# Performance work log

Hardware: AMD Instinct MI355X
Metric: run time of the kernel (lower is better)

The kernel has to match this reference:

```python
import jax, jax.numpy as jnp
import numpy as np

ALPHA = 0.2      # LeakyReLU negative slope
NEG_BIG = -9e15  # mask value from the original module


def setup_inputs() -> dict:
    key = jax.random.key(0)
    kx, ka, kW, ka1, ka2, kb = jax.random.split(key, 6)
    B, N, F_in, F_out = 8, 2048, 256, 128
    x = jax.random.normal(kx, (B, N, F_in), dtype=jnp.float32)
    adj = (jax.random.uniform(ka, (B, N, N)) < 0.1).astype(jnp.float32)
    adj = adj.at[:, jnp.arange(N), jnp.arange(N)].set(1.0)
    # parameters (xavier-uniform-ish scaling)
    W = jax.random.normal(kW, (F_out, F_in), dtype=jnp.float32) * np.sqrt(2.0 / (F_in + F_out))
    a1 = jax.random.normal(ka1, (F_out,), dtype=jnp.float32) * np.sqrt(2.0 / (2 * F_out + 1))
    a2 = jax.random.normal(ka2, (F_out,), dtype=jnp.float32) * np.sqrt(2.0 / (2 * F_out + 1))
    a_b = jax.random.normal(kb, (1,), dtype=jnp.float32) * 0.01
    return {"x": x, "adj": adj, "W": W, "a1": a1, "a2": a2, "a_b": a_b}


def reference(x, adj, W, a1, a2, a_b):
    # h = W(input): [B, N, F_out]
    h = jnp.einsum('bnf,of->bno', x, W)
    # a([h_i, h_j]) == a1.h_i + a2.h_j + bias  (exact decomposition of the concat)
    s1 = h @ a1  # [B, N] contribution of row-repeated node i
    s2 = h @ a2  # [B, N] contribution of tiled node j
    e = jax.nn.leaky_relu(s1[:, :, None] + s2[:, None, :] + a_b[0], negative_slope=ALPHA)  # [B,N,N]
    att = jnp.where(adj > 0, e, NEG_BIG)
    att = jax.nn.softmax(att, axis=1)  # softmax over dim=1, as in the original
    # dropout is a no-op in eval mode
    att = att * adj
    h_prime = jnp.einsum('bij,bjo->bio', att, h)
    return jax.nn.elu(h_prime)  # concat=True -> ELU
```

## Files before the change

### kernel.cpp

```cpp
#include <hip/hip_runtime.h>
#include <stdint.h>

typedef unsigned int  uint32;
typedef unsigned long long u64;

#define L2E 1.44269504088896340736f

typedef float f32x4 __attribute__((ext_vector_type(4)));
typedef short bf16x8 __attribute__((ext_vector_type(8)));

__device__ __forceinline__ unsigned short f2bf(float f){
  uint32 u = __float_as_uint(f);
  u += 0x7fffu + ((u >> 16) & 1u);
  return (unsigned short)(u >> 16);
}


__global__ __launch_bounds__(256) void k_h(const float* __restrict__ x,
                                           const float* __restrict__ W,
                                           const float* __restrict__ a1,
                                           const float* __restrict__ a2,
                                           const float* __restrict__ ab,
                                           float* __restrict__ h,
                                           float* __restrict__ E1,
                                           float* __restrict__ E2p){
  __shared__ unsigned short xs[2][64][72];
  __shared__ unsigned short wsm[2][128][72];
  const int tid = threadIdx.x;
  const int wv = tid >> 6, lane = tid & 63;
  const int r = lane & 15, kg = lane >> 4;
  const int row0 = blockIdx.x * 64;

  f32x4 acc[8];
  #pragma unroll
  for (int of = 0; of < 8; ++of) acc[of] = (f32x4){0.f,0.f,0.f,0.f};

  for (int kc = 0; kc < 4; ++kc){
    if (kc) __syncthreads();
    #pragma unroll
    for (int it = 0; it < 4; ++it){
      int idx = tid + it * 256;
      int row = idx >> 4, f = (idx & 15) * 4;
      float4 v = *(const float4*)(x + (size_t)(row0 + row) * 256 + kc * 64 + f);
      ushort4 hi, lo;
      { unsigned short hh = f2bf(v.x); float rr = v.x - __uint_as_float(((uint32)hh)<<16); hi.x = hh; lo.x = f2bf(rr); }
      { unsigned short hh = f2bf(v.y); float rr = v.y - __uint_as_float(((uint32)hh)<<16); hi.y = hh; lo.y = f2bf(rr); }
      { unsigned short hh = f2bf(v.z); float rr = v.z - __uint_as_float(((uint32)hh)<<16); hi.z = hh; lo.z = f2bf(rr); }
      { unsigned short hh = f2bf(v.w); float rr = v.w - __uint_as_float(((uint32)hh)<<16); hi.w = hh; lo.w = f2bf(rr); }
      *(ushort4*)&xs[0][row][f] = hi;
      *(ushort4*)&xs[1][row][f] = lo;
    }
    #pragma unroll
    for (int it = 0; it < 8; ++it){
      int idx = tid + it * 256;
      int o = idx >> 4, f = (idx & 15) * 4;
      float4 v = *(const float4*)(W + (size_t)o * 256 + kc * 64 + f);
      ushort4 hi, lo;
      { unsigned short hh = f2bf(v.x); float rr = v.x - __uint_as_float(((uint32)hh)<<16); hi.x = hh; lo.x = f2bf(rr); }
      { unsigned short hh = f2bf(v.y); float rr = v.y - __uint_as_float(((uint32)hh)<<16); hi.y = hh; lo.y = f2bf(rr); }
      { unsigned short hh = f2bf(v.z); float rr = v.z - __uint_as_float(((uint32)hh)<<16); hi.z = hh; lo.z = f2bf(rr); }
      { unsigned short hh = f2bf(v.w); float rr = v.w - __uint_as_float(((uint32)hh)<<16); hi.w = hh; lo.w = f2bf(rr); }
      *(ushort4*)&wsm[0][o][f] = hi;
      *(ushort4*)&wsm[1][o][f] = lo;
    }
    __syncthreads();
    #pragma unroll
    for (int kk = 0; kk < 2; ++kk){
      bf16x8 ah = *(const bf16x8*)&xs[0][wv*16 + r][kk*32 + kg*8];
      bf16x8 al = *(const bf16x8*)&xs[1][wv*16 + r][kk*32 + kg*8];
      #pragma unroll
      for (int of = 0; of < 8; ++of){
        bf16x8 bh = *(const bf16x8*)&wsm[0][of*16 + r][kk*32 + kg*8];
        bf16x8 bl = *(const bf16x8*)&wsm[1][of*16 + r][kk*32 + kg*8];
        acc[of] = __builtin_amdgcn_mfma_f32_16x16x32_bf16(ah, bh, acc[of], 0, 0, 0);
        acc[of] = __builtin_amdgcn_mfma_f32_16x16x32_bf16(ah, bl, acc[of], 0, 0, 0);
        acc[of] = __builtin_amdgcn_mfma_f32_16x16x32_bf16(al, bh, acc[of], 0, 0, 0);
      }
    }
  }
  #pragma unroll
  for (int of = 0; of < 8; ++of)
    #pragma unroll
    for (int q = 0; q < 4; ++q)
      h[(size_t)(row0 + wv*16 + kg*4 + q) * 128 + of*16 + r] = acc[of][q];

  float p1[4] = {0,0,0,0}, p2[4] = {0,0,0,0};
  #pragma unroll
  for (int of = 0; of < 8; ++of){
    float w1 = a1[of*16 + r], w2 = a2[of*16 + r];
    #pragma unroll
    for (int q = 0; q < 4; ++q){
      p1[q] = fmaf(acc[of][q], w1, p1[q]);
      p2[q] = fmaf(acc[of][q], w2, p2[q]);
    }
  }
  #pragma unroll
  for (int off = 8; off; off >>= 1)
    #pragma unroll
    for (int q = 0; q < 4; ++q){
      p1[q] += __shfl_xor(p1[q], off);
      p2[q] += __shfl_xor(p2[q], off);
    }
  if (r == 0){
    float abv = ab[0];
    #pragma unroll
    for (int q = 0; q < 4; ++q){
      int row = row0 + wv*16 + kg*4 + q;
      E1[row] = p1[q] * L2E;
      int bb = row >> 11, j = row & 2047;
      int kp = (j & ~255) + (j & 3) * 64 + ((j & 255) >> 2);
      E2p[bb * 2048 + kp] = (p2[q] + abv) * L2E;
    }
  }
}

__global__ __launch_bounds__(256) void k_dm(const float* __restrict__ adj,
                                            const float* __restrict__ E1,
                                            const float* __restrict__ E2p,
                                            float* __restrict__ denomP,
                                            u64* __restrict__ mask){
  __shared__ float red[4][256];
  const int b = blockIdx.z, Q = blockIdx.x, ic = blockIdx.y;
  const int wv = threadIdx.x >> 6, lane = threadIdx.x & 63;
  const int Jbase = Q * 256;
  const int row0 = ic * 64 + wv * 16;
  const int grow0 = b * 2048 + row0;

  const f32x4* ap = (const f32x4*)(adj + (size_t)grow0 * 2048 + Jbase) + lane;
  u64* mp = mask + (size_t)grow0 * 32 + Q * 4;

  float e2v[4];
  #pragma unroll
  for (int p = 0; p < 4; ++p)
    e2v[p] = E2p[b * 2048 + Q * 256 + p * 64 + lane];

  float e1r[16];
  #pragma unroll
  for (int q = 0; q < 4; ++q){
    float4 t = *(const float4*)(E1 + grow0 + q * 4);
    e1r[q*4+0] = t.x; e1r[q*4+1] = t.y; e1r[q*4+2] = t.z; e1r[q*4+3] = t.w;
  }

  float ds0 = 0.f, ds1 = 0.f, ds2 = 0.f, ds3 = 0.f;

  #pragma unroll
  for (int rr = 0; rr < 16; ++rr){
    f32x4 av = __builtin_nontemporal_load(ap + (size_t)rr * 512);
    const float e1 = e1r[rr];
    float t0 = e1 + e2v[0]; t0 = fmaxf(t0, 0.2f * t0);
    float t1 = e1 + e2v[1]; t1 = fmaxf(t1, 0.2f * t1);
    float t2 = e1 + e2v[2]; t2 = fmaxf(t2, 0.2f * t2);
    float t3 = e1 + e2v[3]; t3 = fmaxf(t3, 0.2f * t3);
    ds0 = fmaf(av[0], __builtin_amdgcn_exp2f(t0), ds0);
    ds1 = fmaf(av[1], __builtin_amdgcn_exp2f(t1), ds1);
    ds2 = fmaf(av[2], __builtin_amdgcn_exp2f(t2), ds2);
    ds3 = fmaf(av[3], __builtin_amdgcn_exp2f(t3), ds3);
    u64 b0 = __ballot(av[0] != 0.f);
    u64 b1 = __ballot(av[1] != 0.f);
    u64 b2 = __ballot(av[2] != 0.f);
    u64 b3 = __ballot(av[3] != 0.f);
    if (lane == 0){
      ulonglong2* dst = (ulonglong2*)(mp + (size_t)rr * 32);
      dst[0] = (ulonglong2){b0, b1};
      dst[1] = (ulonglong2){b2, b3};
    }
  }

  *(float4*)&red[wv][lane * 4] = (float4){ds0, ds1, ds2, ds3};
  __syncthreads();
  const int t = threadIdx.x;
  denomP[(size_t)ic * 16384 + b * 2048 + Jbase + t] = red[0][t] + red[1][t] + red[2][t] + red[3][t];
}

__global__ __launch_bounds__(256) void k_gt(const float* __restrict__ h,
                                            const float* __restrict__ denomP,
                                            unsigned short* __restrict__ gTp){
  __shared__ float hl[8464];
  __shared__ float rrec[256];
  const int b = blockIdx.z, Q = blockIdx.x, ot = blockIdx.y;
  const int o0 = ot * 32;
  const int tid = threadIdx.x;

  {
    float d = 0.f;
    #pragma unroll
    for (int icc = 0; icc < 32; ++icc)
      d += denomP[(size_t)icc * 16384 + b * 2048 + Q * 256 + tid];
    rrec[tid] = 1.0f / d;
  }
  __syncthreads();

  #pragma unroll
  for (int it = 0; it < 8; ++it){
    int idx = tid + it * 256;
    int j = idx >> 3, f = idx & 7;
    float4 v = *(const float4*)(h + (size_t)(b * 2048 + Q * 256 + j) * 128 + o0 + f * 4);
    float rc = rrec[j];
    int base = j * 33 + (j >> 4) + f * 4;
    hl[base + 0] = v.x * rc;
    hl[base + 1] = v.y * rc;
    hl[base + 2] = v.z * rc;
    hl[base + 3] = v.w * rc;
  }
  __syncthreads();

  const int u  = tid & 127;
  const int fh = tid >> 7;
  const int lane = u >> 1;
  const int e0 = (u & 1) * 4;
  const int orow_r = lane & 15;
  const int kgrp = lane >> 4;
  #pragma unroll
  for (int it = 0; it < 8; ++it){
    int f  = it * 2 + fh;
    int kb = f >> 1, sl = f & 1;
    int orow = sl * 16 + orow_r;
    int klb = kb * 32 + kgrp * 8 + e0;
    ushort4 uu;
    { int kl = klb + 0; int jl = 4 * (kl & 63) + (kl >> 6); uu.x = f2bf(hl[jl * 33 + (jl >> 4) + orow]); }
    { int kl = klb + 1; int jl = 4 * (kl & 63) + (kl >> 6); uu.y = f2bf(hl[jl * 33 + (jl >> 4) + orow]); }
    { int kl = klb + 2; int jl = 4 * (kl & 63) + (kl >> 6); uu.z = f2bf(hl[jl * 33 + (jl >> 4) + orow]); }
    { int kl = klb + 3; int jl = 4 * (kl & 63) + (kl >> 6); uu.w = f2bf(hl[jl * 33 + (jl >> 4) + orow]); }
    size_t dst = ((size_t)((b * 64 + Q * 8 + kb) * 8 + (ot * 2 + sl))) * 512 + lane * 8 + e0;
    *(ushort4*)(gTp + dst) = uu;
  }
}

__global__ __launch_bounds__(256) void k_main(const float* __restrict__ E1,
                                              const float* __restrict__ E2p,
                                              const uint32* __restrict__ mask32,
                                              const unsigned short* __restrict__ gTp,
                                              float* __restrict__ out){
  __shared__ float cmb[4][32][129];
  const int b  = blockIdx.y;
  const int ib = blockIdx.x;
  const int wv = threadIdx.x >> 6, lane = threadIdx.x & 63;
  const int r  = lane & 15, kg = lane >> 4;
  const int gi0 = b * 2048 + ib * 32 + r;
  const float e1_0 = E1[gi0];
  const float e1_1 = E1[gi0 + 16];
  const uint32* m0 = mask32 + (size_t)gi0 * 64;
  const uint32* m1 = mask32 + (size_t)(gi0 + 16) * 64;

  f32x4 acc[2][8];
  #pragma unroll
  for (int si = 0; si < 2; ++si)
    #pragma unroll
    for (int so = 0; so < 8; ++so)
      acc[si][so] = (f32x4){0.f, 0.f, 0.f, 0.f};

  const int k0 = wv * 512, k1 = k0 + 512;
  for (int kk = k0; kk < k1; kk += 32){
    const int j0 = kk + kg * 8;
    const float4 eA = *(const float4*)(E2p + b * 2048 + j0);
    const float4 eB = *(const float4*)(E2p + b * 2048 + j0 + 4);
    const uint32 bits0 = (m0[kk >> 5] >> (kg * 8)) & 0xffu;
    const uint32 bits1 = (m1[kk >> 5] >> (kg * 8)) & 0xffu;
    float e2v[8] = {eA.x, eA.y, eA.z, eA.w, eB.x, eB.y, eB.z, eB.w};

    union { uint32 u[4]; bf16x8 v; } af0, af1;
    #pragma unroll
    for (int p = 0; p < 4; ++p){
      {
        float t0 = e1_0 + e2v[2*p];     t0 = fmaxf(t0, 0.2f * t0);
        float t1 = e1_0 + e2v[2*p+1];   t1 = fmaxf(t1, 0.2f * t1);
        float x0 = ((bits0 >> (2*p))   & 1u) ? __builtin_amdgcn_exp2f(t0) : 0.f;
        float x1 = ((bits0 >> (2*p+1)) & 1u) ? __builtin_amdgcn_exp2f(t1) : 0.f;
        uint32 u0 = __float_as_uint(x0); u0 = (u0 + 0x7fffu + ((u0 >> 16) & 1u)) >> 16;
        uint32 u1 = __float_as_uint(x1); u1 = (u1 + 0x7fffu + ((u1 >> 16) & 1u)) & 0xffff0000u;
        af0.u[p] = u0 | u1;
      }
      {
        float t0 = e1_1 + e2v[2*p];     t0 = fmaxf(t0, 0.2f * t0);
        float t1 = e1_1 + e2v[2*p+1];   t1 = fmaxf(t1, 0.2f * t1);
        float x0 = ((bits1 >> (2*p))   & 1u) ? __builtin_amdgcn_exp2f(t0) : 0.f;
        float x1 = ((bits1 >> (2*p+1)) & 1u) ? __builtin_amdgcn_exp2f(t1) : 0.f;
        uint32 u0 = __float_as_uint(x0); u0 = (u0 + 0x7fffu + ((u0 >> 16) & 1u)) >> 16;
        uint32 u1 = __float_as_uint(x1); u1 = (u1 + 0x7fffu + ((u1 >> 16) & 1u)) & 0xffff0000u;
        af1.u[p] = u0 | u1;
      }
    }
    const unsigned short* gk = gTp + ((size_t)(b * 64 + (kk >> 5)) * 8) * 512 + lane * 8;
    #pragma unroll
    for (int so = 0; so < 8; ++so){
      bf16x8 bfr = *(const bf16x8*)(gk + so * 512);
      acc[0][so] = __builtin_amdgcn_mfma_f32_16x16x32_bf16(af0.v, bfr, acc[0][so], 0, 0, 0);
      acc[1][so] = __builtin_amdgcn_mfma_f32_16x16x32_bf16(af1.v, bfr, acc[1][so], 0, 0, 0);
    }
  }

  #pragma unroll
  for (int si = 0; si < 2; ++si)
    #pragma unroll
    for (int so = 0; so < 8; ++so)
      #pragma unroll
      for (int q = 0; q < 4; ++q){
        int il = si * 16 + kg * 4 + q;
        int o  = so * 16 + r;
        cmb[wv][il][o] = acc[si][so][q];
      }
  __syncthreads();
  for (int e = threadIdx.x; e < 4096; e += 256){
    int i = e >> 7, o = e & 127;
    float v = cmb[0][i][o] + cmb[1][i][o] + cmb[2][i][o] + cmb[3][i][o];
    float res = v > 0.f ? v : (__builtin_amdgcn_exp2f(v * L2E) - 1.0f);
    out[(size_t)(b * 2048 + ib * 32 + i) * 128 + o] = res;
  }
}

extern "C" void kernel_launch(void* const* d_in, const int* in_sizes, int n_in,
                              void* d_out, int out_size, void* d_ws, size_t ws_size,
                              hipStream_t stream){
  const float* x   = (const float*)d_in[0];
  const float* adj = (const float*)d_in[1];
  const float* W   = (const float*)d_in[2];
  const float* a1  = (const float*)d_in[3];
  const float* a2  = (const float*)d_in[4];
  const float* ab  = (const float*)d_in[5];
  float* out = (float*)d_out;

  const size_t WS_NEEDED = 19005440;
  if (ws_size < WS_NEEDED) return;

  char* ws = (char*)d_ws;
  float* h      = (float*)(ws);
  float* E1     = (float*)(ws + 8388608);
  float* E2p    = (float*)(ws + 8454144);
  float* denomP = (float*)(ws + 8519680);
  u64*   mask   = (u64*)  (ws + 10616832);
  unsigned short* gTp = (unsigned short*)(ws + 14811136);

  k_h  <<<256, 256, 0, stream>>>(x, W, a1, a2, ab, h, E1, E2p);
  k_dm <<<dim3(8, 32, 8), 256, 0, stream>>>(adj, E1, E2p, denomP, mask);
  k_gt <<<dim3(8, 4, 8), 256, 0, stream>>>(h, denomP, gTp);
  k_main<<<dim3(64, 8), 256, 0, stream>>>(E1, E2p, (const uint32*)mask, gTp, out);
}
```

Measured before the change: 77.92 us.

## Give each k_dm block 256 rows and batch adjacency loads eight at a time

The k_dm column-sum/mask kernel now has each wave process 64 rows instead of 16, so the grid shrinks from 32 to 8 row-chunks and the partial-denominator buffer and its reduction in k_gt shrink to match. Adjacency rows are loaded in groups of eight per loop iteration to keep more memory requests in flight, and the nontemporal load hint is dropped. This cuts the partial-sum traffic and the k_gt reduction work, but leaves 512 blocks instead of 2048 to cover the large adjacency read, which may lower memory-level parallelism.

```diff
diff --git a/kernel.cpp b/kernel.cpp
--- a/kernel.cpp
+++ b/kernel.cpp
@@ -123,46 +123,44 @@
   const int b = blockIdx.z, Q = blockIdx.x, ic = blockIdx.y;
   const int wv = threadIdx.x >> 6, lane = threadIdx.x & 63;
   const int Jbase = Q * 256;
-  const int row0 = ic * 64 + wv * 16;
-  const int grow0 = b * 2048 + row0;
-
-  const f32x4* ap = (const f32x4*)(adj + (size_t)grow0 * 2048 + Jbase) + lane;
-  u64* mp = mask + (size_t)grow0 * 32 + Q * 4;
+  const int row0 = ic * 256 + wv * 64;
+
+  const float* e1p = E1 + b * 2048 + row0;
+  const f32x4* ap = (const f32x4*)(adj + (size_t)(b * 2048 + row0) * 2048 + Jbase) + lane;
+  u64* mp = mask + (size_t)(b * 2048 + row0) * 32 + Q * 4;
 
   float e2v[4];
   #pragma unroll
   for (int p = 0; p < 4; ++p)
     e2v[p] = E2p[b * 2048 + Q * 256 + p * 64 + lane];
 
-  float e1r[16];
-  #pragma unroll
-  for (int q = 0; q < 4; ++q){
-    float4 t = *(const float4*)(E1 + grow0 + q * 4);
-    e1r[q*4+0] = t.x; e1r[q*4+1] = t.y; e1r[q*4+2] = t.z; e1r[q*4+3] = t.w;
-  }
-
   float ds0 = 0.f, ds1 = 0.f, ds2 = 0.f, ds3 = 0.f;
 
-  #pragma unroll
-  for (int rr = 0; rr < 16; ++rr){
-    f32x4 av = __builtin_nontemporal_load(ap + (size_t)rr * 512);
-    const float e1 = e1r[rr];
-    float t0 = e1 + e2v[0]; t0 = fmaxf(t0, 0.2f * t0);
-    float t1 = e1 + e2v[1]; t1 = fmaxf(t1, 0.2f * t1);
-    float t2 = e1 + e2v[2]; t2 = fmaxf(t2, 0.2f * t2);
-    float t3 = e1 + e2v[3]; t3 = fmaxf(t3, 0.2f * t3);
-    ds0 = fmaf(av[0], __builtin_amdgcn_exp2f(t0), ds0);
-    ds1 = fmaf(av[1], __builtin_amdgcn_exp2f(t1), ds1);
-    ds2 = fmaf(av[2], __builtin_amdgcn_exp2f(t2), ds2);
-    ds3 = fmaf(av[3], __builtin_amdgcn_exp2f(t3), ds3);
-    u64 b0 = __ballot(av[0] != 0.f);
-    u64 b1 = __ballot(av[1] != 0.f);
-    u64 b2 = __ballot(av[2] != 0.f);
-    u64 b3 = __ballot(av[3] != 0.f);
-    if (lane == 0){
-      ulonglong2* dst = (ulonglong2*)(mp + (size_t)rr * 32);
-      dst[0] = (ulonglong2){b0, b1};
-      dst[1] = (ulonglong2){b2, b3};
+  for (int r0 = 0; r0 < 64; r0 += 8){
+    f32x4 av[8];
+    #pragma unroll
+    for (int u = 0; u < 8; ++u)
+      av[u] = ap[(size_t)(r0 + u) * 512];
+    #pragma unroll
+    for (int u = 0; u < 8; ++u){
+      const float e1 = e1p[r0 + u];
+      float t0 = e1 + e2v[0]; t0 = fmaxf(t0, 0.2f * t0);
+      float t1 = e1 + e2v[1]; t1 = fmaxf(t1, 0.2f * t1);
+      float t2 = e1 + e2v[2]; t2 = fmaxf(t2, 0.2f * t2);
+      float t3 = e1 + e2v[3]; t3 = fmaxf(t3, 0.2f * t3);
+      ds0 = fmaf(av[u][0], __builtin_amdgcn_exp2f(t0), ds0);
+      ds1 = fmaf(av[u][1], __builtin_amdgcn_exp2f(t1), ds1);
+      ds2 = fmaf(av[u][2], __builtin_amdgcn_exp2f(t2), ds2);
+      ds3 = fmaf(av[u][3], __builtin_amdgcn_exp2f(t3), ds3);
+      u64 b0 = __ballot(av[u][0] != 0.f);
+      u64 b1 = __ballot(av[u][1] != 0.f);
+      u64 b2 = __ballot(av[u][2] != 0.f);
+      u64 b3 = __ballot(av[u][3] != 0.f);
+      if (lane == 0){
+        ulonglong2* dst = (ulonglong2*)(mp + (size_t)(r0 + u) * 32);
+        dst[0] = (ulonglong2){b0, b1};
+        dst[1] = (ulonglong2){b2, b3};
+      }
     }
   }
 
@@ -184,7 +182,7 @@
   {
     float d = 0.f;
     #pragma unroll
-    for (int icc = 0; icc < 32; ++icc)
+    for (int icc = 0; icc < 8; ++icc)
       d += denomP[(size_t)icc * 16384 + b * 2048 + Q * 256 + tid];
     rrec[tid] = 1.0f / d;
   }
@@ -319,7 +317,7 @@
   const float* ab  = (const float*)d_in[5];
   float* out = (float*)d_out;
 
-  const size_t WS_NEEDED = 19005440;
+  const size_t WS_NEEDED = 17432576;
   if (ws_size < WS_NEEDED) return;
 
   char* ws = (char*)d_ws;
@@ -327,11 +325,11 @@
   float* E1     = (float*)(ws + 8388608);
   float* E2p    = (float*)(ws + 8454144);
   float* denomP = (float*)(ws + 8519680);
-  u64*   mask   = (u64*)  (ws + 10616832);
-  unsigned short* gTp = (unsigned short*)(ws + 14811136);
+  u64*   mask   = (u64*)  (ws + 9043968);
+  unsigned short* gTp = (unsigned short*)(ws + 13238272);
 
   k_h  <<<256, 256, 0, stream>>>(x, W, a1, a2, ab, h, E1, E2p);
-  k_dm <<<dim3(8, 32, 8), 256, 0, stream>>>(adj, E1, E2p, denomP, mask);
+  k_dm <<<dim3(8, 8, 8), 256, 0, stream>>>(adj, E1, E2p, denomP, mask);
   k_gt <<<dim3(8, 4, 8), 256, 0, stream>>>(h, denomP, gTp);
   k_main<<<dim3(64, 8), 256, 0, stream>>>(E1, E2p, (const uint32*)mask, gTp, out);
 }
```

Measured after the change: 68.68 us, median of 2. 1.13x faster.

## Split adjacency bitmask build from denominator; compute column sums from bitmask

Applied to the files above, without the earlier changes.

Replaces the fused adjacency-scan kernel with two kernels. A pure mask builder streams the dense adjacency once and writes the bitmask. A new denominator kernel then reads the compact bitmask plus E1/E2 to compute the column softmax sums in fewer partial chunks. The mask kernel launches before the projection kernel, so the dense adj read no longer waits on the projection. In exchange it adds a launch and recomputes exp for every (i,j) pair from the bitmask. It also changes the partial-sum layout that the gather kernel reads.

```diff
diff --git a/kernel.cpp b/kernel.cpp
--- a/kernel.cpp
+++ b/kernel.cpp
@@ -15,6 +15,32 @@
   return (unsigned short)(u >> 16);
 }
 
+
+__global__ __launch_bounds__(256) void k_mask(const float* __restrict__ adj,
+                                              u64* __restrict__ mask){
+  const int bid = blockIdx.x;
+  const int wv = threadIdx.x >> 6, lane = threadIdx.x & 63;
+  const int row0 = bid * 16 + wv * 4;
+  const f32x4* ap = (const f32x4*)(adj + (size_t)row0 * 2048) + lane;
+  u64* mp = mask + (size_t)row0 * 32;
+
+  #pragma unroll
+  for (int rr = 0; rr < 4; ++rr){
+    #pragma unroll
+    for (int c = 0; c < 8; ++c){
+      f32x4 av = ap[(size_t)rr * 512 + c * 64];
+      u64 b0 = __ballot(av[0] != 0.f);
+      u64 b1 = __ballot(av[1] != 0.f);
+      u64 b2 = __ballot(av[2] != 0.f);
+      u64 b3 = __ballot(av[3] != 0.f);
+      if (lane == 0){
+        ulonglong2* dst = (ulonglong2*)(mp + (size_t)rr * 32 + c * 4);
+        dst[0] = (ulonglong2){b0, b1};
+        dst[1] = (ulonglong2){b2, b3};
+      }
+    }
+  }
+}
 
 __global__ __launch_bounds__(256) void k_h(const float* __restrict__ x,
                                            const float* __restrict__ W,
@@ -114,66 +140,33 @@
   }
 }
 
-__global__ __launch_bounds__(256) void k_dm(const float* __restrict__ adj,
-                                            const float* __restrict__ E1,
-                                            const float* __restrict__ E2p,
-                                            float* __restrict__ denomP,
-                                            u64* __restrict__ mask){
-  __shared__ float red[4][256];
-  const int b = blockIdx.z, Q = blockIdx.x, ic = blockIdx.y;
+__global__ __launch_bounds__(256) void k_den(const u64* __restrict__ mask,
+                                             const float* __restrict__ E1,
+                                             const float* __restrict__ E2p,
+                                             float* __restrict__ denomK){
+  const int wg = blockIdx.x, ch = blockIdx.y, b = blockIdx.z;
   const int wv = threadIdx.x >> 6, lane = threadIdx.x & 63;
-  const int Jbase = Q * 256;
-  const int row0 = ic * 64 + wv * 16;
-  const int grow0 = b * 2048 + row0;
-
-  const f32x4* ap = (const f32x4*)(adj + (size_t)grow0 * 2048 + Jbase) + lane;
-  u64* mp = mask + (size_t)grow0 * 32 + Q * 4;
-
-  float e2v[4];
-  #pragma unroll
-  for (int p = 0; p < 4; ++p)
-    e2v[p] = E2p[b * 2048 + Q * 256 + p * 64 + lane];
-
-  float e1r[16];
-  #pragma unroll
-  for (int q = 0; q < 4; ++q){
-    float4 t = *(const float4*)(E1 + grow0 + q * 4);
-    e1r[q*4+0] = t.x; e1r[q*4+1] = t.y; e1r[q*4+2] = t.z; e1r[q*4+3] = t.w;
-  }
-
-  float ds0 = 0.f, ds1 = 0.f, ds2 = 0.f, ds3 = 0.f;
-
-  #pragma unroll
-  for (int rr = 0; rr < 16; ++rr){
-    f32x4 av = __builtin_nontemporal_load(ap + (size_t)rr * 512);
-    const float e1 = e1r[rr];
-    float t0 = e1 + e2v[0]; t0 = fmaxf(t0, 0.2f * t0);
-    float t1 = e1 + e2v[1]; t1 = fmaxf(t1, 0.2f * t1);
-    float t2 = e1 + e2v[2]; t2 = fmaxf(t2, 0.2f * t2);
-    float t3 = e1 + e2v[3]; t3 = fmaxf(t3, 0.2f * t3);
-    ds0 = fmaf(av[0], __builtin_amdgcn_exp2f(t0), ds0);
-    ds1 = fmaf(av[1], __builtin_amdgcn_exp2f(t1), ds1);
-    ds2 = fmaf(av[2], __builtin_amdgcn_exp2f(t2), ds2);
-    ds3 = fmaf(av[3], __builtin_amdgcn_exp2f(t3), ds3);
-    u64 b0 = __ballot(av[0] != 0.f);
-    u64 b1 = __ballot(av[1] != 0.f);
-    u64 b2 = __ballot(av[2] != 0.f);
-    u64 b3 = __ballot(av[3] != 0.f);
-    if (lane == 0){
-      ulonglong2* dst = (ulonglong2*)(mp + (size_t)rr * 32);
-      dst[0] = (ulonglong2){b0, b1};
-      dst[1] = (ulonglong2){b2, b3};
-    }
-  }
-
-  *(float4*)&red[wv][lane * 4] = (float4){ds0, ds1, ds2, ds3};
-  __syncthreads();
-  const int t = threadIdx.x;
-  denomP[(size_t)ic * 16384 + b * 2048 + Jbase + t] = red[0][t] + red[1][t] + red[2][t] + red[3][t];
+  const int w = wg * 4 + wv;
+  const float e2 = E2p[b * 2048 + w * 64 + lane];
+  const u64 lmask = 1ull << lane;
+  const float* e1p = E1 + b * 2048 + ch * 128;
+  const u64* mpp = mask + (size_t)(b * 2048 + ch * 128) * 32 + w;
+
+  float acc = 0.f;
+  #pragma unroll 8
+  for (int i = 0; i < 128; ++i){
+    u64 wb = mpp[(size_t)i * 32];
+    float e1 = e1p[i];
+    float t = e1 + e2;
+    t = fmaxf(t, 0.2f * t);
+    float v = __builtin_amdgcn_exp2f(t);
+    acc += (wb & lmask) ? v : 0.f;
+  }
+  denomK[(size_t)ch * 16384 + b * 2048 + w * 64 + lane] = acc;
 }
 
 __global__ __launch_bounds__(256) void k_gt(const float* __restrict__ h,
-                                            const float* __restrict__ denomP,
+                                            const float* __restrict__ denomK,
                                             unsigned short* __restrict__ gTp){
   __shared__ float hl[8464];
   __shared__ float rrec[256];
@@ -182,10 +175,11 @@
   const int tid = threadIdx.x;
 
   {
+    const int kpl = (tid & 3) * 64 + (tid >> 2);
     float d = 0.f;
     #pragma unroll
-    for (int icc = 0; icc < 32; ++icc)
-      d += denomP[(size_t)icc * 16384 + b * 2048 + Q * 256 + tid];
+    for (int ch = 0; ch < 16; ++ch)
+      d += denomK[(size_t)ch * 16384 + b * 2048 + Q * 256 + kpl];
     rrec[tid] = 1.0f / d;
   }
   __syncthreads();
@@ -319,19 +313,20 @@
   const float* ab  = (const float*)d_in[5];
   float* out = (float*)d_out;
 
-  const size_t WS_NEEDED = 19005440;
+  const size_t WS_NEEDED = 17956864;
   if (ws_size < WS_NEEDED) return;
 
   char* ws = (char*)d_ws;
   float* h      = (float*)(ws);
   float* E1     = (float*)(ws + 8388608);
   float* E2p    = (float*)(ws + 8454144);
-  float* denomP = (float*)(ws + 8519680);
-  u64*   mask   = (u64*)  (ws + 10616832);
-  unsigned short* gTp = (unsigned short*)(ws + 14811136);
-
-  k_h  <<<256, 256, 0, stream>>>(x, W, a1, a2, ab, h, E1, E2p);
-  k_dm <<<dim3(8, 32, 8), 256, 0, stream>>>(adj, E1, E2p, denomP, mask);
-  k_gt <<<dim3(8, 4, 8), 256, 0, stream>>>(h, denomP, gTp);
+  float* denomK = (float*)(ws + 8519680);
+  u64*   mask   = (u64*)  (ws + 9568256);
+  unsigned short* gTp = (unsigned short*)(ws + 13762560);
+
+  k_mask<<<1024, 256, 0, stream>>>(adj, mask);
+  k_h   <<<256, 256, 0, stream>>>(x, W, a1, a2, ab, h, E1, E2p);
+  k_den <<<dim3(8, 16, 8), 256, 0, stream>>>(mask, E1, E2p, denomK);
+  k_gt  <<<dim3(8, 4, 8), 256, 0, stream>>>(h, denomK, gTp);
   k_main<<<dim3(64, 8), 256, 0, stream>>>(E1, E2p, (const uint32*)mask, gTp, out);
 }
```

New measurement: 84.21 us. 1.08x slower.
